# Kernel optimization log

Measured on AMD Instinct MI355X. Metric: run time of the kernel, lower is better.

## Reference

```python
import jax, jax.numpy as jnp
import numpy as np

N_HEAD = 16
D_MODEL = 1024
BATCH = 2
SEQ = 2048


def setup_inputs() -> dict:
    key = jax.random.key(0)
    ks = jax.random.split(key, 12)
    s = 0.02
    inp = {
        "q": jax.random.normal(ks[0], (BATCH, SEQ, D_MODEL), jnp.float32),
        "k": jax.random.normal(ks[1], (BATCH, SEQ, D_MODEL), jnp.float32),
        "v": jax.random.normal(ks[2], (BATCH, SEQ, D_MODEL), jnp.float32),
        "Wq": jax.random.normal(ks[3], (D_MODEL, D_MODEL), jnp.float32) * s,
        "bq": jnp.zeros((D_MODEL,), jnp.float32),
        "Wk": jax.random.normal(ks[4], (D_MODEL, D_MODEL), jnp.float32) * s,
        "bk": jnp.zeros((D_MODEL,), jnp.float32),
        "Wv": jax.random.normal(ks[5], (D_MODEL, D_MODEL), jnp.float32) * s,
        "bv": jnp.zeros((D_MODEL,), jnp.float32),
        "Wo": jax.random.normal(ks[6], (D_MODEL, D_MODEL), jnp.float32) * s,
        "bo": jnp.zeros((D_MODEL,), jnp.float32),
    }
    return inp


def reference(q, k, v, Wq, bq, Wk, bk, Wv, bv, Wo, bo):
    B, S, D = q.shape
    H = N_HEAD
    Dh = D // H
    # NOTE: faithful to source -- scale uses d_model, not head_dim
    scale = D ** 0.5

    # torch nn.Linear: y = x @ W.T + b
    qw = q @ Wq.T + bq
    kw = k @ Wk.T + bk
    vw = v @ Wv.T + bv

    # chunk(n_head, dim=-1) == contiguous last-dim head slices
    qh = qw.reshape(B, S, H, Dh)
    kh = kw.reshape(B, S, H, Dh)
    vh = vw.reshape(B, S, H, Dh)

    scores = jnp.einsum("bshd,bthd->bhst", qh, kh) / scale  # [B,H,S,S]
    causal = jnp.triu(jnp.ones((S, S), dtype=bool), k=1)
    scores = jnp.where(causal, -jnp.inf, scores)
    p = jax.nn.softmax(scores, axis=-1)
    out = jnp.einsum("bhst,bthd->bshd", p, vh).reshape(B, S, D)
    return out @ Wo.T + bo
```

## Files before the change

kernel.cpp:

```cpp
#include <hip/hip_runtime.h>
#include <hip/hip_bf16.h>
#include <stdint.h>
#include <type_traits>

#define NHEAD  16
#define DMODEL 1024
#define BATCH  2
#define SEQ    2048
#define DH     64
#define MROWS  (BATCH*SEQ)

typedef __attribute__((ext_vector_type(8))) short bf16x8;
typedef __attribute__((ext_vector_type(4))) float f32x4;

__device__ inline short f2bs(float f) {
    __hip_bfloat16 h = __float2bfloat16(f);
    return *reinterpret_cast<short*>(&h);
}

__device__ inline uint32_t pk2(float lo, float hi) {
    return (uint32_t)(uint16_t)f2bs(lo) | ((uint32_t)(uint16_t)f2bs(hi) << 16);
}

__device__ inline void async16(const void* g, void* l) {
    __builtin_amdgcn_global_load_lds(
        (__attribute__((address_space(1))) void*)g,
        (__attribute__((address_space(3))) void*)l, 16, 0, 0);
}

__global__ __launch_bounds__(256)
void convert_all(const float* __restrict__ Wq, const float* __restrict__ Wk,
                 const float* __restrict__ Wv, const float* __restrict__ Wo,
                 const float* __restrict__ q, const float* __restrict__ k,
                 const float* __restrict__ v,
                 __hip_bfloat16* __restrict__ Wqkv, __hip_bfloat16* __restrict__ Wob,
                 __hip_bfloat16* __restrict__ qb, __hip_bfloat16* __restrict__ kb,
                 __hip_bfloat16* __restrict__ vb)
{
    const int idx = (blockIdx.x * 256 + threadIdx.x) * 8;
    const float* src;
    __hip_bfloat16* dst;
    if (idx < 3 * 1048576) {
        const int g = idx >> 20;
        src = (g == 0 ? Wq : (g == 1 ? Wk : Wv)) + (idx & 1048575);
        dst = Wqkv + idx;
    } else if (idx < 4 * 1048576) {
        src = Wo + (idx - 3 * 1048576);
        dst = Wob + (idx - 3 * 1048576);
    } else if (idx < 8 * 1048576) {
        src = q + (idx - 4 * 1048576);
        dst = qb + (idx - 4 * 1048576);
    } else if (idx < 12 * 1048576) {
        src = k + (idx - 8 * 1048576);
        dst = kb + (idx - 8 * 1048576);
    } else {
        src = v + (idx - 12 * 1048576);
        dst = vb + (idx - 12 * 1048576);
    }
    float4 f0 = *(const float4*)src;
    float4 f1 = *(const float4*)(src + 4);
    short o[8];
    o[0] = f2bs(f0.x); o[1] = f2bs(f0.y); o[2] = f2bs(f0.z); o[3] = f2bs(f0.w);
    o[4] = f2bs(f1.x); o[5] = f2bs(f1.y); o[6] = f2bs(f1.z); o[7] = f2bs(f1.w);
    *(uint4*)dst = *(uint4*)o;
}

__global__ __launch_bounds__(256)
void transpose_v(const __hip_bfloat16* __restrict__ vp, __hip_bfloat16* __restrict__ vt)
{
    __shared__ short L[64 * 72];
    const int t  = threadIdx.x;
    const int st = blockIdx.x & 63;
    const int ht = blockIdx.x >> 6;
    {
        const int r = t >> 2, cs = (t & 3) * 16;
        const __hip_bfloat16* src = vp + (size_t)(st * 64 + r) * DMODEL + ht * 64 + cs;
        *(uint4*)&L[r * 72 + cs]     = *(const uint4*)src;
        *(uint4*)&L[r * 72 + cs + 8] = *(const uint4*)(src + 8);
    }
    __syncthreads();
    const int d  = t >> 2;
    const int ss = (t & 3) * 16;
    const int m0 = st * 64;
    const int b  = m0 >> 11;
    const int s0 = (m0 & 2047) + ss;
    short o[16];
#pragma unroll
    for (int i = 0; i < 16; i++) o[i] = L[(ss + i) * 72 + d];
    __hip_bfloat16* dst = vt + ((size_t)((b * NHEAD + ht) * DH + d)) * SEQ + s0;
    *(uint4*)dst       = *(uint4*)&o[0];
    *(uint4*)(dst + 8) = *(uint4*)&o[8];
}

template <typename TC, bool DBUF>
__global__ __launch_bounds__(256, DBUF ? 2 : 3)
void gemm_bt(const __hip_bfloat16* __restrict__ A0, const __hip_bfloat16* __restrict__ A1,
             const __hip_bfloat16* __restrict__ A2,
             const __hip_bfloat16* __restrict__ B,
             const float* __restrict__ b0, const float* __restrict__ b1, const float* __restrict__ b2,
             TC* __restrict__ C0, TC* __restrict__ C1, TC* __restrict__ C2,
             float os0)
{
    __shared__ short As[DBUF ? 2 : 1][128 * 64];
    __shared__ short Bs[DBUF ? 2 : 1][128 * 64];

    const int t    = threadIdx.x;
    const int lane = t & 63;
    const int w    = t >> 6;
    const int wm   = (w >> 1) * 64;
    const int wn   = (w & 1) * 64;
    const int quad = lane >> 4;
    const int l16  = lane & 15;

    const int g = blockIdx.x >> 3;
    const __hip_bfloat16* A = (g == 0) ? A0 : (g == 1 ? A1 : A2);
    const float* bias       = (g == 0) ? b0 : (g == 1 ? b1 : b2);
    TC* C                   = (g == 0) ? C0 : (g == 1 ? C1 : C2);
    const float osc         = (g == 0) ? os0 : 1.f;
    const int    bm  = blockIdx.y * 128;
    const int    bnl = (blockIdx.x & 7) * 128;
    const size_t bng = (size_t)blockIdx.x * 128;

    f32x4 acc[4][4];
#pragma unroll
    for (int i = 0; i < 4; i++)
#pragma unroll
        for (int j = 0; j < 4; j++)
            acc[i][j] = (f32x4){0.f, 0.f, 0.f, 0.f};

    auto STAGEG = [&](int kt, int buf) {
#pragma unroll
        for (int i = 0; i < 4; i++) {
            const int p  = i * 256 + t;
            const int br = p >> 3;
            const int c8 = ((p & 7) - br) & 7;
            async16(B + (bng + br) * DMODEL + kt + c8 * 8,
                    &Bs[buf][(i * 256 + (w << 6)) * 8]);
            async16(A + (size_t)(bm + br) * DMODEL + kt + c8 * 8,
                    &As[buf][(i * 256 + (w << 6)) * 8]);
        }
    };

    int cur = 0;
    if constexpr (DBUF) STAGEG(0, 0);

    for (int kt = 0; kt < DMODEL; kt += 64) {
        __syncthreads();
        if constexpr (DBUF) {
            if (kt + 64 < DMODEL) STAGEG(kt + 64, cur ^ 1);
        } else {
            STAGEG(kt, 0);
            __syncthreads();
        }

#pragma unroll
        for (int kk = 0; kk < 2; kk++) {
            bf16x8 af[4], bf[4];
#pragma unroll
            for (int mi = 0; mi < 4; mi++) {
                const int row = wm + mi * 16 + l16;
                const int pc  = ((quad + 4 * kk) + row) & 7;
                af[mi] = *(const bf16x8*)&As[cur][row * 64 + pc * 8];
            }
#pragma unroll
            for (int ni = 0; ni < 4; ni++) {
                const int row = wn + ni * 16 + l16;
                const int pc  = ((quad + 4 * kk) + row) & 7;
                bf[ni] = *(const bf16x8*)&Bs[cur][row * 64 + pc * 8];
            }
#pragma unroll
            for (int mi = 0; mi < 4; mi++)
#pragma unroll
                for (int ni = 0; ni < 4; ni++)
                    acc[mi][ni] = __builtin_amdgcn_mfma_f32_16x16x32_bf16(
                        af[mi], bf[ni], acc[mi][ni], 0, 0, 0);
        }
        if constexpr (DBUF) cur ^= 1;
    }

#pragma unroll
    for (int mi = 0; mi < 4; mi++) {
#pragma unroll
        for (int ni = 0; ni < 4; ni++) {
            const int row0 = bm + wm + mi * 16 + quad * 4;
            const int coll = bnl + wn + ni * 16 + l16;
            const float bb = bias[coll];
#pragma unroll
            for (int r = 0; r < 4; r++) {
                const float val = (acc[mi][ni][r] + bb) * osc;
                if constexpr (std::is_same<TC, float>::value)
                    C[(size_t)(row0 + r) * DMODEL + coll] = val;
                else
                    C[(size_t)(row0 + r) * DMODEL + coll] = __float2bfloat16(val);
            }
        }
    }
}

__global__ __launch_bounds__(256, 4)
void attn_flash_wg(const __hip_bfloat16* __restrict__ qp,
                   const __hip_bfloat16* __restrict__ kp,
                   const __hip_bfloat16* __restrict__ vt,
                   __hip_bfloat16* __restrict__ po0,
                   __hip_bfloat16* __restrict__ po1,
                   float* __restrict__ ml)
{
    __shared__ short Ks[2][64 * 64];
    __shared__ short Vs[2][64 * 64];

    const int t    = threadIdx.x;
    const int lane = t & 63;
    const int w    = t >> 6;
    const int l16  = lane & 15;
    const int quad = lane >> 4;

    const int bh   = blockIdx.x & 31;
    const int cidx = 79 - ((int)blockIdx.x >> 5);
    int st, c;
    if (cidx < 8)       { st = cidx; c = 0; }
    else if (cidx < 24) { const int u = cidx - 8;  st = 8 + (u >> 1); c = u & 1; }
    else if (cidx < 48) { const int u = cidx - 24; const int q3 = u / 3; st = 16 + q3; c = u - 3 * q3; }
    else                { const int u = cidx - 48; st = 24 + (u >> 2); c = u & 3; }
    const int bid = bh * 80 +
        ((st < 8) ? st : (st < 16) ? 8 + 2 * (st - 8) : (st < 24) ? 24 + 3 * (st - 16)
                                                      : 48 + 4 * (st - 24)) + c;
    const int b = bh >> 4;
    const int h = bh & 15;

    const __hip_bfloat16* qptr =
        qp + (size_t)(b * SEQ + 64 * st + 16 * w + l16) * DMODEL + h * DH + quad * 8;
    bf16x8 aq0 = *(const bf16x8*)qptr;
    bf16x8 aq1 = *(const bf16x8*)(qptr + 32);

    float l = 0.f;
    f32x4 oc[4];
#pragma unroll
    for (int dt = 0; dt < 4; dt++) oc[dt] = (f32x4){0.f, 0.f, 0.f, 0.f};

    const __hip_bfloat16* kbase = kp + (size_t)(b * SEQ) * DMODEL + h * DH;
    const __hip_bfloat16* vbase = vt + (size_t)(bh * DH) * SEQ;

    const int kmax   = 64 * st + 64;
    const int key_lo = 512 * c;
    const int nst    = (min(key_lo + 512, kmax) - key_lo) >> 6;
    const int rql    = 16 * w + l16;

    auto STAGE = [&](int js, int buf) {
        const int key0 = key_lo + (js << 6);
#pragma unroll
        for (int i = 0; i < 2; i++) {
            const int p    = i * 256 + t;
            const int row  = p >> 3;
            const int c8   = ((p & 7) - row) & 7;
            const int krow = (row & 3) | ((row & 12) << 1) | ((row & 16) << 1)
                           | ((row & 32) >> 3);
            async16(kbase + (size_t)(key0 + krow) * DMODEL + c8 * 8,
                    &Ks[buf][(i * 256 + (w << 6)) * 8]);
            async16(vbase + (size_t)row * SEQ + key0 + c8 * 8,
                    &Vs[buf][(i * 256 + (w << 6)) * 8]);
        }
    };

    STAGE(0, 0);
    int cur = 0;

    for (int js = 0; js < nst; ++js) {
        __syncthreads();
        if (js + 1 < nst) STAGE(js + 1, cur ^ 1);

        const int key0 = key_lo + (js << 6);

        f32x4 sc[4];
        __builtin_amdgcn_s_setprio(1);
#pragma unroll
        for (int ct = 0; ct < 4; ct++) {
            const int row = 16 * ct + l16;
            bf16x8 bk0 = *(const bf16x8*)&Ks[cur][row * 64 + ((quad + row) & 7) * 8];
            bf16x8 bk1 = *(const bf16x8*)&Ks[cur][row * 64 + ((quad + 4 + row) & 7) * 8];
            sc[ct] = __builtin_amdgcn_mfma_f32_16x16x32_bf16(
                bk0, aq0, (f32x4){0.f, 0.f, 0.f, 0.f}, 0, 0, 0);
            sc[ct] = __builtin_amdgcn_mfma_f32_16x16x32_bf16(bk1, aq1, sc[ct], 0, 0, 0);
        }
        __builtin_amdgcn_s_setprio(0);

        if (key0 == 64 * st) {
#pragma unroll
            for (int ct = 0; ct < 4; ct++)
#pragma unroll
                for (int r = 0; r < 4; r++) {
                    const int km = 8 * quad + 32 * (ct & 1) + 4 * (ct >> 1) + r;
                    if (km > rql) sc[ct][r] = -__builtin_inff();
                }
        }

        float psum = 0.f;
#pragma unroll
        for (int ct = 0; ct < 4; ct++)
#pragma unroll
            for (int r = 0; r < 4; r++) {
                const float e = exp2f(sc[ct][r]);
                sc[ct][r] = e;
                psum += e;
            }

        union U8 { uint32_t u[4]; bf16x8 v; } ap0u, ap1u;
        ap0u.u[0] = pk2(sc[0][0], sc[0][1]);
        ap0u.u[1] = pk2(sc[0][2], sc[0][3]);
        ap0u.u[2] = pk2(sc[2][0], sc[2][1]);
        ap0u.u[3] = pk2(sc[2][2], sc[2][3]);
        ap1u.u[0] = pk2(sc[1][0], sc[1][1]);
        ap1u.u[1] = pk2(sc[1][2], sc[1][3]);
        ap1u.u[2] = pk2(sc[3][0], sc[3][1]);
        ap1u.u[3] = pk2(sc[3][2], sc[3][3]);

        __builtin_amdgcn_s_setprio(1);
#pragma unroll
        for (int dt = 0; dt < 4; dt++) {
            const int row = 16 * dt + l16;
            bf16x8 bv0 = *(const bf16x8*)&Vs[cur][row * 64 + ((quad + row) & 7) * 8];
            bf16x8 bv1 = *(const bf16x8*)&Vs[cur][row * 64 + ((quad + 4 + row) & 7) * 8];
            oc[dt] = __builtin_amdgcn_mfma_f32_16x16x32_bf16(ap0u.v, bv0, oc[dt], 0, 0, 0);
            oc[dt] = __builtin_amdgcn_mfma_f32_16x16x32_bf16(ap1u.v, bv1, oc[dt], 0, 0, 0);
        }
        __builtin_amdgcn_s_setprio(0);

        psum += __shfl_xor(psum, 16);
        psum += __shfl_xor(psum, 32);
        l += psum;
        cur ^= 1;
    }

    __hip_bfloat16* pp = (bid < 2048) ? po0 + (size_t)bid * 4096
                                      : po1 + (size_t)(bid - 2048) * 4096;
#pragma unroll
    for (int r = 0; r < 4; r++) {
        const int row = 16 * w + quad * 4 + r;
#pragma unroll
        for (int dt = 0; dt < 4; dt++)
            pp[row * 64 + 16 * dt + l16] = __float2bfloat16(oc[dt][r]);
    }
    if (quad == 0) {
        ml[(size_t)bid * 128 + 16 * w + l16]      = 0.f;
        ml[(size_t)bid * 128 + 64 + 16 * w + l16] = l;
    }
}

__global__ __launch_bounds__(256)
void attn_reduce(const __hip_bfloat16* __restrict__ po0, const __hip_bfloat16* __restrict__ po1,
                 const float* __restrict__ ml, __hip_bfloat16* __restrict__ ao)
{
    const int col = threadIdx.x & 63;
    const int r0  = threadIdx.x >> 6;
    const int bh  = blockIdx.x >> 5;
    const int st  = blockIdx.x & 31;
    const int nch = (st >> 3) + 1;
    const int pre = (st < 8) ? st : (st < 16) ? 8 + 2 * (st - 8)
                  : (st < 24) ? 24 + 3 * (st - 16) : 48 + 4 * (st - 24);
    const int bid0 = bh * 80 + pre;
    const int b = bh >> 4;
    const int h = bh & 15;

    for (int i = 0; i < 16; i++) {
        const int row = r0 + 4 * i;
        float M = -__builtin_inff();
        for (int cc = 0; cc < nch; cc++)
            M = fmaxf(M, ml[(size_t)(bid0 + cc) * 128 + row]);
        float L = 0.f, O = 0.f;
        for (int cc = 0; cc < nch; cc++) {
            const int bidc = bid0 + cc;
            const float wgt = exp2f(ml[(size_t)bidc * 128 + row] - M);
            L += ml[(size_t)bidc * 128 + 64 + row] * wgt;
            const __hip_bfloat16* pp = (bidc < 2048) ? po0 + (size_t)bidc * 4096
                                                     : po1 + (size_t)(bidc - 2048) * 4096;
            O += wgt * __bfloat162float(pp[row * 64 + col]);
        }
        ao[(size_t)(b * SEQ + 64 * st + row) * DMODEL + h * DH + col] =
            __float2bfloat16(O / L);
    }
}

extern "C" void kernel_launch(void* const* d_in, const int* in_sizes, int n_in,
                              void* d_out, int out_size, void* d_ws, size_t ws_size,
                              hipStream_t stream) {
    const float* q  = (const float*)d_in[0];
    const float* k  = (const float*)d_in[1];
    const float* v  = (const float*)d_in[2];
    const float* Wq = (const float*)d_in[3];
    const float* bq = (const float*)d_in[4];
    const float* Wk = (const float*)d_in[5];
    const float* bk = (const float*)d_in[6];
    const float* Wv = (const float*)d_in[7];
    const float* bv = (const float*)d_in[8];
    const float* Wo = (const float*)d_in[9];
    const float* bo = (const float*)d_in[10];
    float* out = (float*)d_out;

    __hip_bfloat16* Wqkv = (__hip_bfloat16*)d_ws;
    __hip_bfloat16* Wob  = Wqkv + (size_t)3072 * 1024;
    __hip_bfloat16* qp   = Wob  + (size_t)1024 * 1024;
    __hip_bfloat16* kp   = qp   + (size_t)MROWS * DMODEL;
    __hip_bfloat16* vp   = kp   + (size_t)MROWS * DMODEL;
    __hip_bfloat16* vb   = vp   + (size_t)MROWS * DMODEL;
    float*          mlb  = (float*)(vb + (size_t)MROWS * DMODEL);
    __hip_bfloat16* qb   = (__hip_bfloat16*)d_out;
    __hip_bfloat16* kb   = qb + (size_t)MROWS * DMODEL;
    __hip_bfloat16* vtg  = vb;
    __hip_bfloat16* ao   = vp;
    __hip_bfloat16* po0  = (__hip_bfloat16*)d_out;
    __hip_bfloat16* po1  = Wqkv;

    const float qscale = 0.03125f * 1.44269504088896340736f;

    hipLaunchKernelGGL(convert_all, dim3(8192), dim3(256), 0, stream,
                       Wq, Wk, Wv, Wo, q, k, v, Wqkv, Wob, qb, kb, vb);

    hipLaunchKernelGGL((gemm_bt<__hip_bfloat16, false>), dim3(24, 32), dim3(256), 0, stream,
                       qb, kb, vb, Wqkv, bq, bk, bv, qp, kp, vp, qscale);

    hipLaunchKernelGGL(transpose_v, dim3(1024), dim3(256), 0, stream, vp, vtg);

    hipLaunchKernelGGL(attn_flash_wg, dim3(2560), dim3(256), 0, stream,
                       qp, kp, vtg, po0, po1, mlb);

    hipLaunchKernelGGL(attn_reduce, dim3(1024), dim3(256), 0, stream,
                       po0, po1, mlb, ao);

    hipLaunchKernelGGL((gemm_bt<float, true>), dim3(8, 32), dim3(256), 0, stream,
                       ao, ao, ao, Wob, bo, bo, bo, out, out, out, 1.0f);
}
```

Before: 258.3 us.

## Use 128-row query blocks with 8 waves sharing each K/V tile

The attention kernel grows from 64 to 128 query rows per workgroup, using 512 threads (8 waves), so each staged K/V tile in LDS is reused by twice as many waves. The grid is halved, the chunk-to-query-block mapping and the partial-output/stat layouts are rescaled, and the reduce kernel is adapted to match. Staging now issues one async load per thread per tile with incrementally advanced pointers, and causal masking covers the two diagonal tiles. This trades fewer, larger workgroups (lower parallelism, possibly lower occupancy under launch_bounds(512,8)) for halved K/V global traffic and fewer barriers per unit of work.

```diff
diff --git a/kernel.cpp b/kernel.cpp
--- a/kernel.cpp
+++ b/kernel.cpp
@@ -9,6 +9,7 @@
 #define SEQ    2048
 #define DH     64
 #define MROWS  (BATCH*SEQ)
+#define QBLK   128
 
 typedef __attribute__((ext_vector_type(8))) short bf16x8;
 typedef __attribute__((ext_vector_type(4))) float f32x4;
@@ -197,7 +198,7 @@
     }
 }
 
-__global__ __launch_bounds__(256, 4)
+__global__ __launch_bounds__(512, 8)
 void attn_flash_wg(const __hip_bfloat16* __restrict__ qp,
                    const __hip_bfloat16* __restrict__ kp,
                    const __hip_bfloat16* __restrict__ vt,
@@ -215,20 +216,20 @@
     const int quad = lane >> 4;
 
     const int bh   = blockIdx.x & 31;
-    const int cidx = 79 - ((int)blockIdx.x >> 5);
+    const int cidx = 39 - ((int)blockIdx.x >> 5);
     int st, c;
-    if (cidx < 8)       { st = cidx; c = 0; }
-    else if (cidx < 24) { const int u = cidx - 8;  st = 8 + (u >> 1); c = u & 1; }
-    else if (cidx < 48) { const int u = cidx - 24; const int q3 = u / 3; st = 16 + q3; c = u - 3 * q3; }
-    else                { const int u = cidx - 48; st = 24 + (u >> 2); c = u & 3; }
-    const int bid = bh * 80 +
-        ((st < 8) ? st : (st < 16) ? 8 + 2 * (st - 8) : (st < 24) ? 24 + 3 * (st - 16)
-                                                      : 48 + 4 * (st - 24)) + c;
+    if (cidx < 4)       { st = cidx; c = 0; }
+    else if (cidx < 12) { const int u = cidx - 4;  st = 4 + (u >> 1); c = u & 1; }
+    else if (cidx < 24) { const int u = cidx - 12; const int q3 = u / 3; st = 8 + q3; c = u - 3 * q3; }
+    else                { const int u = cidx - 24; st = 12 + (u >> 2); c = u & 3; }
+    const int pre = (st < 4) ? st : (st < 8) ? 4 + 2 * (st - 4)
+                  : (st < 12) ? 12 + 3 * (st - 8) : 24 + 4 * (st - 12);
+    const int bid = bh * 40 + pre + c;
     const int b = bh >> 4;
     const int h = bh & 15;
 
     const __hip_bfloat16* qptr =
-        qp + (size_t)(b * SEQ + 64 * st + 16 * w + l16) * DMODEL + h * DH + quad * 8;
+        qp + (size_t)(b * SEQ + QBLK * st + 16 * w + l16) * DMODEL + h * DH + quad * 8;
     bf16x8 aq0 = *(const bf16x8*)qptr;
     bf16x8 aq1 = *(const bf16x8*)(qptr + 32);
 
@@ -240,35 +241,33 @@
     const __hip_bfloat16* kbase = kp + (size_t)(b * SEQ) * DMODEL + h * DH;
     const __hip_bfloat16* vbase = vt + (size_t)(bh * DH) * SEQ;
 
-    const int kmax   = 64 * st + 64;
+    const int kmax   = QBLK * st + QBLK;
     const int key_lo = 512 * c;
     const int nst    = (min(key_lo + 512, kmax) - key_lo) >> 6;
     const int rql    = 16 * w + l16;
 
-    auto STAGE = [&](int js, int buf) {
-        const int key0 = key_lo + (js << 6);
-#pragma unroll
-        for (int i = 0; i < 2; i++) {
-            const int p    = i * 256 + t;
-            const int row  = p >> 3;
-            const int c8   = ((p & 7) - row) & 7;
-            const int krow = (row & 3) | ((row & 12) << 1) | ((row & 16) << 1)
-                           | ((row & 32) >> 3);
-            async16(kbase + (size_t)(key0 + krow) * DMODEL + c8 * 8,
-                    &Ks[buf][(i * 256 + (w << 6)) * 8]);
-            async16(vbase + (size_t)row * SEQ + key0 + c8 * 8,
-                    &Vs[buf][(i * 256 + (w << 6)) * 8]);
-        }
-    };
-
-    STAGE(0, 0);
+    const int srow = t >> 3;
+    const int c8   = ((t & 7) - srow) & 7;
+    const int krow = (srow & 3) | ((srow & 12) << 1) | ((srow & 16) << 1) | ((srow & 32) >> 3);
+    const __hip_bfloat16* ksrc = kbase + (size_t)(key_lo + krow) * DMODEL + c8 * 8;
+    const __hip_bfloat16* vsrc = vbase + (size_t)srow * SEQ + key_lo + c8 * 8;
+
+    short* kd[2] = { &Ks[0][(w << 6) * 8], &Ks[1][(w << 6) * 8] };
+    short* vd[2] = { &Vs[0][(w << 6) * 8], &Vs[1][(w << 6) * 8] };
+
+    async16(ksrc, kd[0]);
+    async16(vsrc, vd[0]);
     int cur = 0;
+    int key0 = key_lo;
 
     for (int js = 0; js < nst; ++js) {
         __syncthreads();
-        if (js + 1 < nst) STAGE(js + 1, cur ^ 1);
-
-        const int key0 = key_lo + (js << 6);
+        if (js + 1 < nst) {
+            ksrc += (size_t)64 * DMODEL;
+            vsrc += 64;
+            async16(ksrc, kd[cur ^ 1]);
+            async16(vsrc, vd[cur ^ 1]);
+        }
 
         f32x4 sc[4];
         __builtin_amdgcn_s_setprio(1);
@@ -283,13 +282,14 @@
         }
         __builtin_amdgcn_s_setprio(0);
 
-        if (key0 == 64 * st) {
+        if (key0 > kmax - 129) {
+            const int kd0 = key0 - (kmax - QBLK);
 #pragma unroll
             for (int ct = 0; ct < 4; ct++)
 #pragma unroll
                 for (int r = 0; r < 4; r++) {
                     const int km = 8 * quad + 32 * (ct & 1) + 4 * (ct >> 1) + r;
-                    if (km > rql) sc[ct][r] = -__builtin_inff();
+                    if (kd0 + km > rql) sc[ct][r] = -__builtin_inff();
                 }
         }
 
@@ -327,11 +327,12 @@
         psum += __shfl_xor(psum, 16);
         psum += __shfl_xor(psum, 32);
         l += psum;
+        key0 += 64;
         cur ^= 1;
     }
 
-    __hip_bfloat16* pp = (bid < 2048) ? po0 + (size_t)bid * 4096
-                                      : po1 + (size_t)(bid - 2048) * 4096;
+    __hip_bfloat16* pp = (bid < 1024) ? po0 + (size_t)bid * 8192
+                                      : po1 + (size_t)(bid - 1024) * 8192;
 #pragma unroll
     for (int r = 0; r < 4; r++) {
         const int row = 16 * w + quad * 4 + r;
@@ -340,8 +341,8 @@
             pp[row * 64 + 16 * dt + l16] = __float2bfloat16(oc[dt][r]);
     }
     if (quad == 0) {
-        ml[(size_t)bid * 128 + 16 * w + l16]      = 0.f;
-        ml[(size_t)bid * 128 + 64 + 16 * w + l16] = l;
+        ml[(size_t)bid * 256 + 16 * w + l16]       = 0.f;
+        ml[(size_t)bid * 256 + 128 + 16 * w + l16] = l;
     }
 }
 
@@ -351,30 +352,30 @@
 {
     const int col = threadIdx.x & 63;
     const int r0  = threadIdx.x >> 6;
-    const int bh  = blockIdx.x >> 5;
-    const int st  = blockIdx.x & 31;
-    const int nch = (st >> 3) + 1;
-    const int pre = (st < 8) ? st : (st < 16) ? 8 + 2 * (st - 8)
-                  : (st < 24) ? 24 + 3 * (st - 16) : 48 + 4 * (st - 24);
-    const int bid0 = bh * 80 + pre;
+    const int bh  = blockIdx.x >> 4;
+    const int st  = blockIdx.x & 15;
+    const int nch = (st >> 2) + 1;
+    const int pre = (st < 4) ? st : (st < 8) ? 4 + 2 * (st - 4)
+                  : (st < 12) ? 12 + 3 * (st - 8) : 24 + 4 * (st - 12);
+    const int bid0 = bh * 40 + pre;
     const int b = bh >> 4;
     const int h = bh & 15;
 
-    for (int i = 0; i < 16; i++) {
+    for (int i = 0; i < 32; i++) {
         const int row = r0 + 4 * i;
         float M = -__builtin_inff();
         for (int cc = 0; cc < nch; cc++)
-            M = fmaxf(M, ml[(size_t)(bid0 + cc) * 128 + row]);
+            M = fmaxf(M, ml[(size_t)(bid0 + cc) * 256 + row]);
         float L = 0.f, O = 0.f;
         for (int cc = 0; cc < nch; cc++) {
             const int bidc = bid0 + cc;
-            const float wgt = exp2f(ml[(size_t)bidc * 128 + row] - M);
-            L += ml[(size_t)bidc * 128 + 64 + row] * wgt;
-            const __hip_bfloat16* pp = (bidc < 2048) ? po0 + (size_t)bidc * 4096
-                                                     : po1 + (size_t)(bidc - 2048) * 4096;
+            const float wgt = exp2f(ml[(size_t)bidc * 256 + row] - M);
+            L += ml[(size_t)bidc * 256 + 128 + row] * wgt;
+            const __hip_bfloat16* pp = (bidc < 1024) ? po0 + (size_t)bidc * 8192
+                                                     : po1 + (size_t)(bidc - 1024) * 8192;
             O += wgt * __bfloat162float(pp[row * 64 + col]);
         }
-        ao[(size_t)(b * SEQ + 64 * st + row) * DMODEL + h * DH + col] =
+        ao[(size_t)(b * SEQ + QBLK * st + row) * DMODEL + h * DH + col] =
             __float2bfloat16(O / L);
     }
 }
@@ -419,10 +420,10 @@
 
     hipLaunchKernelGGL(transpose_v, dim3(1024), dim3(256), 0, stream, vp, vtg);
 
-    hipLaunchKernelGGL(attn_flash_wg, dim3(2560), dim3(256), 0, stream,
+    hipLaunchKernelGGL(attn_flash_wg, dim3(1280), dim3(512), 0, stream,
                        qp, kp, vtg, po0, po1, mlb);
 
-    hipLaunchKernelGGL(attn_reduce, dim3(1024), dim3(256), 0, stream,
+    hipLaunchKernelGGL(attn_reduce, dim3(512), dim3(256), 0, stream,
                        po0, po1, mlb, ao);
 
     hipLaunchKernelGGL((gemm_bt<float, true>), dim3(8, 32), dim3(256), 0, stream,
```

Measured after the change: 313.0 us. 1.21x slower.
